# Kernel optimization log

Measured on AMD Instinct MI355X. Metric: run time of the kernel, lower is better.

The kernel has to match this reference:

```python
import jax, jax.numpy as jnp
import numpy as np

N, L, H, V = 64, 512, 1024, 32000


def setup_inputs() -> dict:
    key = jax.random.key(0)
    k1, k2, k3, k4, k5, k6 = jax.random.split(key, 6)
    s = 1.0 / np.sqrt(H)
    return {
        "x": jax.random.randint(k1, (N, L), 0, V, dtype=jnp.int32),
        "emb": jax.random.normal(k2, (V, H), dtype=jnp.float32) * 0.02,
        "W_hh_w": jax.random.normal(k3, (H, H), dtype=jnp.float32) * s,
        "W_hh_b": jax.random.normal(k4, (H,), dtype=jnp.float32) * s,
        "W_xh_w": jax.random.normal(k5, (H, H), dtype=jnp.float32) * s,
        "W_xh_b": jax.random.normal(k6, (H,), dtype=jnp.float32) * s,
    }


def reference(x, emb, W_hh_w, W_hh_b, W_xh_w, W_xh_b):
    # h_t = tanh(W_hh h_{t-1} + b_hh + W_xh e_t + b_xh); returns (N, L, H)
    now = emb[x]                                    # (N, L, H) embedding lookup
    # W_xh part has no recurrence: precompute for all steps at once.
    xh = jnp.einsum("nlh,oh->nlo", now, W_xh_w) + W_xh_b + W_hh_b  # (N, L, H)

    def step(h, xh_t):
        h = jnp.tanh(h @ W_hh_w.T + xh_t)           # (N, H)
        return h, h

    h0 = jnp.zeros((x.shape[0], W_hh_w.shape[0]), dtype=emb.dtype)
    _, memories = jax.lax.scan(step, h0, jnp.swapaxes(xh, 0, 1))  # (L, N, H)
    return jnp.swapaxes(memories, 0, 1)             # (N, L, H)
```

## Files before the change

kernel.cpp:

```cpp
#include <hip/hip_runtime.h>
#include <math.h>

typedef _Float16 half8 __attribute__((ext_vector_type(8)));
typedef _Float16 half4 __attribute__((ext_vector_type(4)));
typedef float floatx4 __attribute__((ext_vector_type(4)));
typedef unsigned long long u64;

#define NB 64
#define LQ 512
#define HD 1024

__device__ inline half8 cvt2(const float4 a, const float4 b) {
  half8 h;
  h[0]=(_Float16)a.x; h[1]=(_Float16)a.y; h[2]=(_Float16)a.z; h[3]=(_Float16)a.w;
  h[4]=(_Float16)b.x; h[5]=(_Float16)b.y; h[6]=(_Float16)b.z; h[7]=(_Float16)b.w;
  return h;
}

__device__ inline floatx4 ld_sc16(const void* p) {
  floatx4 r;
  asm volatile("global_load_dwordx4 %0, %1, off sc0 sc1"
               : "=v"(r) : "v"(p) : "memory");
  return r;
}
__device__ inline void st_sc16(void* p, floatx4 v) {
  asm volatile("global_store_dwordx4 %0, %1, off sc0 sc1"
               :: "v"(p), "v"(v) : "memory");
}
__device__ inline void st_flag(int* p, int v) {
  __hip_atomic_store(p, v, __ATOMIC_RELAXED, __HIP_MEMORY_SCOPE_SYSTEM);
}
__device__ inline void vmcnt0() { asm volatile("s_waitcnt vmcnt(0)" ::: "memory"); }

__device__ inline float ftanh(float x) {
  float e = __expf(2.0f * x);
  return 1.0f - 2.0f / (e + 1.0f);
}

__global__ __launch_bounds__(256) void gemm1_kernel(
    const int* __restrict__ x, const float* __restrict__ emb,
    const float* __restrict__ Wxh, const float* __restrict__ bxh,
    const float* __restrict__ bhh, float* __restrict__ out)
{
  __shared__ alignas(16) _Float16 As[128][72];
  __shared__ alignas(16) _Float16 Bs[128][72];
  const int tid  = threadIdx.x;
  const int lane = tid & 63, wv = tid >> 6;
  const int wm = wv & 1, wn = wv >> 1;
  const int Mbase = blockIdx.x * 128;
  const int Nbase = blockIdx.y * 128;

  const int srow  = tid >> 1;
  const int shalf = tid & 1;
  const size_t erow = (size_t)x[Mbase + srow] * HD;
  const size_t brow = (size_t)(Nbase + srow) * HD;

  floatx4 acc[4][4];
#pragma unroll
  for (int i = 0; i < 4; i++)
#pragma unroll
    for (int j = 0; j < 4; j++) acc[i][j] = (floatx4)0.f;

  for (int c = 0; c < 16; ++c) {
    const int k0 = c * 64 + shalf * 32;
    const float4* ap = (const float4*)(emb + erow + k0);
    const float4* bp = (const float4*)(Wxh + brow + k0);
    float4 av[8], bv[8];
#pragma unroll
    for (int i = 0; i < 8; i++) { av[i] = ap[i]; bv[i] = bp[i]; }
    __syncthreads();
#pragma unroll
    for (int i = 0; i < 4; i++) {
      *(half8*)&As[srow][shalf*32 + i*8] = cvt2(av[2*i], av[2*i+1]);
      *(half8*)&Bs[srow][shalf*32 + i*8] = cvt2(bv[2*i], bv[2*i+1]);
    }
    __syncthreads();
#pragma unroll
    for (int s = 0; s < 2; ++s) {
      const int koff = s*32 + (lane >> 4) * 8;
      half8 af[4], bf[4];
#pragma unroll
      for (int i = 0; i < 4; i++) {
        af[i] = *(const half8*)&As[wm*64 + i*16 + (lane & 15)][koff];
        bf[i] = *(const half8*)&Bs[wn*64 + i*16 + (lane & 15)][koff];
      }
#pragma unroll
      for (int i = 0; i < 4; i++)
#pragma unroll
        for (int j = 0; j < 4; j++)
          acc[i][j] = __builtin_amdgcn_mfma_f32_16x16x32_f16(af[i], bf[j], acc[i][j], 0, 0, 0);
    }
  }
#pragma unroll
  for (int j = 0; j < 4; j++) {
    const int o = Nbase + wn*64 + j*16 + (lane & 15);
    const float bias = bxh[o] + bhh[o];
#pragma unroll
    for (int i = 0; i < 4; i++) {
      const int mb = Mbase + wm*64 + i*16 + ((lane >> 4) * 4);
#pragma unroll
      for (int r = 0; r < 4; r++)
        out[(size_t)(mb + r) * HD + o] = acc[i][j][r] + bias;
    }
  }
}

__global__ __launch_bounds__(256, 1) void rnn_kernel(
    const float* __restrict__ Whh, float* __restrict__ out,
    char* __restrict__ hb, int* __restrict__ flags)
{
  __shared__ alignas(16) _Float16 Ws[32 * 1024];
  __shared__ alignas(16) _Float16 Tls[4 * 16 * 40];
  const int tid = threadIdx.x, lane = tid & 63, w = tid >> 6;
  const int j = blockIdx.x, obase = j * 32;
  const int col = lane & 15, quad = lane >> 4;
  const int wid = j * 4 + w;

  {
    const int o = tid >> 3, t8 = tid & 7;
    const float* src = Whh + (size_t)(obase + o) * HD;
#pragma unroll
    for (int i = 0; i < 16; ++i) {
      const int c16 = t8 * 16 + i;
      float4 v0 = *(const float4*)(src + c16 * 8);
      float4 v1 = *(const float4*)(src + c16 * 8 + 4);
      *(half8*)&Ws[o * 1024 + ((c16 ^ (o & 7)) * 8)] = cvt2(v0, v1);
    }
  }
  __syncthreads();

  const int n = 16 * w + col;
  _Float16* Tw = &Tls[w * 640];
  float* outp = out + (size_t)n * LQ * HD + obase + quad * 4;
  u64* fl64 = (u64*)flags;
  char* hbw = hb + (size_t)w * 32768 + (size_t)lane * 16;

  for (int t = 0; t < LQ; ++t) {
    const float* xp = outp + (size_t)t * HD;
    floatx4 xv0 = *(const floatx4*)xp;
    floatx4 xv1 = *(const floatx4*)(xp + 16);
    floatx4 acc0 = (floatx4)0.f, acc1 = (floatx4)0.f;

    if (t > 0) {
      int spins = 0;
      for (;;) {
        u64 v = __hip_atomic_load(&fl64[lane], __ATOMIC_RELAXED, __HIP_MEMORY_SCOPE_SYSTEM);
        int lo = (int)(unsigned)v, hi = (int)(v >> 32);
        if (__all(lo >= t && hi >= t)) break;
        if (++spins > (1 << 20)) break;
      }

      const char* blk = hbw + (size_t)((t - 1) & 1) * 131072;
      floatx4 hv[32];
#pragma unroll
      for (int c = 0; c < 32; ++c) hv[c] = ld_sc16(blk + c * 1024);

      floatx4 a0a = (floatx4)0.f, a1a = (floatx4)0.f;
      floatx4 a0b = (floatx4)0.f, a1b = (floatx4)0.f;
      asm volatile("s_waitcnt vmcnt(16)" ::: "memory");
      __builtin_amdgcn_sched_barrier(0);
#pragma unroll
      for (int c = 0; c < 16; ++c) {
        const int sw = ((4 * c + quad) ^ (col & 7)) * 8;
        half8 b0 = *(const half8*)&Ws[col * 1024 + sw];
        half8 b1 = *(const half8*)&Ws[(16 + col) * 1024 + sw];
        half8 hf = __builtin_bit_cast(half8, hv[c]);
        a0a = __builtin_amdgcn_mfma_f32_16x16x32_f16(b0, hf, a0a, 0, 0, 0);
        a1a = __builtin_amdgcn_mfma_f32_16x16x32_f16(b1, hf, a1a, 0, 0, 0);
      }
      vmcnt0();
      __builtin_amdgcn_sched_barrier(0);
#pragma unroll
      for (int c = 16; c < 32; ++c) {
        const int sw = ((4 * c + quad) ^ (col & 7)) * 8;
        half8 b0 = *(const half8*)&Ws[col * 1024 + sw];
        half8 b1 = *(const half8*)&Ws[(16 + col) * 1024 + sw];
        half8 hf = __builtin_bit_cast(half8, hv[c]);
        a0b = __builtin_amdgcn_mfma_f32_16x16x32_f16(b0, hf, a0b, 0, 0, 0);
        a1b = __builtin_amdgcn_mfma_f32_16x16x32_f16(b1, hf, a1b, 0, 0, 0);
      }
      acc0 = a0a + a0b;
      acc1 = a1a + a1b;
    }

    floatx4 h0, h1;
    half4 p0, p1;
#pragma unroll
    for (int r = 0; r < 4; ++r) {
      h0[r] = ftanh(acc0[r] + xv0[r]);
      h1[r] = ftanh(acc1[r] + xv1[r]);
      p0[r] = (_Float16)h0[r];
      p1[r] = (_Float16)h1[r];
    }

    *(half4*)&Tw[col * 40 + quad * 4] = p0;
    *(half4*)&Tw[col * 40 + 16 + quad * 4] = p1;
    __builtin_amdgcn_wave_barrier();
    asm volatile("s_waitcnt lgkmcnt(0)" ::: "memory");
    floatx4 myc = *(const floatx4*)&Tw[col * 40 + quad * 8];

    st_sc16(hb + (size_t)(t & 1) * 131072 + (size_t)w * 32768 +
            (size_t)j * 1024 + (size_t)lane * 16, myc);
    vmcnt0();
    if (lane == 0) st_flag(&flags[wid], t + 1);

    float* op = outp + (size_t)t * HD;
    *(floatx4*)op = h0;
    *(floatx4*)(op + 16) = h1;
  }
}

extern "C" void kernel_launch(void* const* d_in, const int* in_sizes, int n_in,
                              void* d_out, int out_size, void* d_ws, size_t ws_size,
                              hipStream_t stream) {
  const int*   x   = (const int*)d_in[0];
  const float* emb = (const float*)d_in[1];
  const float* Whh = (const float*)d_in[2];
  const float* bhh = (const float*)d_in[3];
  const float* Wxh = (const float*)d_in[4];
  const float* bxh = (const float*)d_in[5];
  float* out = (float*)d_out;

  char* hbuf = (char*)d_ws;
  int*  fl   = (int*)((char*)d_ws + 262144);

  gemm1_kernel<<<dim3(256, 8), 256, 0, stream>>>(x, emb, Wxh, bxh, bhh, out);
  rnn_kernel<<<dim3(32), 256, 0, stream>>>(Whh, out, hbuf, fl);
}
```

Measured before the change: 3.526 ms.

## Replace flag-based step sync with sentinel-tagged hidden-state buffers

Drops the per-wave flag publish and spin loop. Consumers instead poll the hidden-state data itself, which is quad-buffered and pre-filled with a sentinel value (initialised in the GEMM kernel and re-armed two steps ahead). Producers write fp16 results straight from registers with two 8-byte system-scope stores, skipping the LDS transpose and the vmcnt wait before the flag store. This removes one round trip (data store, wait, flag store, flag poll) per timestep. The cost is re-polling loads for chunks that are not ready yet, and correctness relies on a real fp16 data pattern never equalling the sentinel and on store ordering within each 4-byte word.

```diff
diff --git a/kernel.cpp b/kernel.cpp
--- a/kernel.cpp
+++ b/kernel.cpp
@@ -4,11 +4,13 @@
 typedef _Float16 half8 __attribute__((ext_vector_type(8)));
 typedef _Float16 half4 __attribute__((ext_vector_type(4)));
 typedef float floatx4 __attribute__((ext_vector_type(4)));
-typedef unsigned long long u64;
+typedef float floatx2 __attribute__((ext_vector_type(2)));
+typedef unsigned int uintx4 __attribute__((ext_vector_type(4)));
 
 #define NB 64
 #define LQ 512
 #define HD 1024
+#define SENT 0x7E7E7E7Eu
 
 __device__ inline half8 cvt2(const float4 a, const float4 b) {
   half8 h;
@@ -17,18 +19,20 @@
   return h;
 }
 
-__device__ inline floatx4 ld_sc16(const void* p) {
+__device__ inline floatx4 ld_sys16(const void* p) {
   floatx4 r;
   asm volatile("global_load_dwordx4 %0, %1, off sc0 sc1"
                : "=v"(r) : "v"(p) : "memory");
   return r;
 }
-__device__ inline void st_sc16(void* p, floatx4 v) {
-  asm volatile("global_store_dwordx4 %0, %1, off sc0 sc1"
+__device__ inline void st_sys8x2(void* p, floatx2 a, floatx2 b) {
+  asm volatile("global_store_dwordx2 %0, %1, off sc0 sc1\n\t"
+               "global_store_dwordx2 %0, %2, off offset:512 sc0 sc1"
+               :: "v"(p), "v"(a), "v"(b) : "memory");
+}
+__device__ inline void st_sys4(void* p, unsigned v) {
+  asm volatile("global_store_dword %0, %1, off sc0 sc1"
                :: "v"(p), "v"(v) : "memory");
-}
-__device__ inline void st_flag(int* p, int v) {
-  __hip_atomic_store(p, v, __ATOMIC_RELAXED, __HIP_MEMORY_SCOPE_SYSTEM);
 }
 __device__ inline void vmcnt0() { asm volatile("s_waitcnt vmcnt(0)" ::: "memory"); }
 
@@ -40,8 +44,15 @@
 __global__ __launch_bounds__(256) void gemm1_kernel(
     const int* __restrict__ x, const float* __restrict__ emb,
     const float* __restrict__ Wxh, const float* __restrict__ bxh,
-    const float* __restrict__ bhh, float* __restrict__ out)
+    const float* __restrict__ bhh, float* __restrict__ out,
+    char* __restrict__ hb)
 {
+  {
+    const int bid = blockIdx.y * gridDim.x + blockIdx.x;
+    if (threadIdx.x < 64)
+      st_sys4((unsigned*)hb + (size_t)bid * 64 + threadIdx.x, SENT);
+  }
+
   __shared__ alignas(16) _Float16 As[128][72];
   __shared__ alignas(16) _Float16 Bs[128][72];
   const int tid  = threadIdx.x;
@@ -107,14 +118,12 @@
 
 __global__ __launch_bounds__(256, 1) void rnn_kernel(
     const float* __restrict__ Whh, float* __restrict__ out,
-    char* __restrict__ hb, int* __restrict__ flags)
+    char* __restrict__ hb)
 {
   __shared__ alignas(16) _Float16 Ws[32 * 1024];
-  __shared__ alignas(16) _Float16 Tls[4 * 16 * 40];
   const int tid = threadIdx.x, lane = tid & 63, w = tid >> 6;
   const int j = blockIdx.x, obase = j * 32;
   const int col = lane & 15, quad = lane >> 4;
-  const int wid = j * 4 + w;
 
   {
     const int o = tid >> 3, t8 = tid & 7;
@@ -130,10 +139,11 @@
   __syncthreads();
 
   const int n = 16 * w + col;
-  _Float16* Tw = &Tls[w * 640];
   float* outp = out + (size_t)n * LQ * HD + obase + quad * 4;
-  u64* fl64 = (u64*)flags;
   char* hbw = hb + (size_t)w * 32768 + (size_t)lane * 16;
+  char* pubb = hb + (size_t)w * 32768 + (size_t)j * 1024 +
+               (size_t)((quad >> 1) * 256 + col * 16 + (quad & 1) * 8);
+  const floatx2 sent2 = __builtin_bit_cast(floatx2, (unsigned long long)SENT << 32 | SENT);
 
   for (int t = 0; t < LQ; ++t) {
     const float* xp = outp + (size_t)t * HD;
@@ -142,42 +152,40 @@
     floatx4 acc0 = (floatx4)0.f, acc1 = (floatx4)0.f;
 
     if (t > 0) {
-      int spins = 0;
-      for (;;) {
-        u64 v = __hip_atomic_load(&fl64[lane], __ATOMIC_RELAXED, __HIP_MEMORY_SCOPE_SYSTEM);
-        int lo = (int)(unsigned)v, hi = (int)(v >> 32);
-        if (__all(lo >= t && hi >= t)) break;
-        if (++spins > (1 << 20)) break;
-      }
-
-      const char* blk = hbw + (size_t)((t - 1) & 1) * 131072;
+      const char* blk = hbw + (size_t)((t - 1) & 3) * 131072;
       floatx4 hv[32];
-#pragma unroll
-      for (int c = 0; c < 32; ++c) hv[c] = ld_sc16(blk + c * 1024);
+      unsigned need = 0xFFFFFFFFu;
+      int sweeps = 0;
+      do {
+#pragma unroll
+        for (int c = 0; c < 32; ++c)
+          if (need & (1u << c)) hv[c] = ld_sys16(blk + c * 1024);
+        vmcnt0();
+        __builtin_amdgcn_sched_barrier(0);
+#pragma unroll
+        for (int c = 0; c < 32; ++c)
+          if (need & (1u << c)) {
+            uintx4 u = __builtin_bit_cast(uintx4, hv[c]);
+            if ((u[0] != SENT) & (u[1] != SENT) & (u[2] != SENT) & (u[3] != SENT))
+              need &= ~(1u << c);
+          }
+      } while (need != 0 && ++sweeps < 4096);
 
       floatx4 a0a = (floatx4)0.f, a1a = (floatx4)0.f;
       floatx4 a0b = (floatx4)0.f, a1b = (floatx4)0.f;
-      asm volatile("s_waitcnt vmcnt(16)" ::: "memory");
-      __builtin_amdgcn_sched_barrier(0);
-#pragma unroll
-      for (int c = 0; c < 16; ++c) {
+#pragma unroll
+      for (int c = 0; c < 32; ++c) {
         const int sw = ((4 * c + quad) ^ (col & 7)) * 8;
         half8 b0 = *(const half8*)&Ws[col * 1024 + sw];
         half8 b1 = *(const half8*)&Ws[(16 + col) * 1024 + sw];
         half8 hf = __builtin_bit_cast(half8, hv[c]);
-        a0a = __builtin_amdgcn_mfma_f32_16x16x32_f16(b0, hf, a0a, 0, 0, 0);
-        a1a = __builtin_amdgcn_mfma_f32_16x16x32_f16(b1, hf, a1a, 0, 0, 0);
-      }
-      vmcnt0();
-      __builtin_amdgcn_sched_barrier(0);
-#pragma unroll
-      for (int c = 16; c < 32; ++c) {
-        const int sw = ((4 * c + quad) ^ (col & 7)) * 8;
-        half8 b0 = *(const half8*)&Ws[col * 1024 + sw];
-        half8 b1 = *(const half8*)&Ws[(16 + col) * 1024 + sw];
-        half8 hf = __builtin_bit_cast(half8, hv[c]);
-        a0b = __builtin_amdgcn_mfma_f32_16x16x32_f16(b0, hf, a0b, 0, 0, 0);
-        a1b = __builtin_amdgcn_mfma_f32_16x16x32_f16(b1, hf, a1b, 0, 0, 0);
+        if (c & 1) {
+          a0b = __builtin_amdgcn_mfma_f32_16x16x32_f16(b0, hf, a0b, 0, 0, 0);
+          a1b = __builtin_amdgcn_mfma_f32_16x16x32_f16(b1, hf, a1b, 0, 0, 0);
+        } else {
+          a0a = __builtin_amdgcn_mfma_f32_16x16x32_f16(b0, hf, a0a, 0, 0, 0);
+          a1a = __builtin_amdgcn_mfma_f32_16x16x32_f16(b1, hf, a1a, 0, 0, 0);
+        }
       }
       acc0 = a0a + a0b;
       acc1 = a1a + a1b;
@@ -193,16 +201,10 @@
       p1[r] = (_Float16)h1[r];
     }
 
-    *(half4*)&Tw[col * 40 + quad * 4] = p0;
-    *(half4*)&Tw[col * 40 + 16 + quad * 4] = p1;
-    __builtin_amdgcn_wave_barrier();
-    asm volatile("s_waitcnt lgkmcnt(0)" ::: "memory");
-    floatx4 myc = *(const floatx4*)&Tw[col * 40 + quad * 8];
-
-    st_sc16(hb + (size_t)(t & 1) * 131072 + (size_t)w * 32768 +
-            (size_t)j * 1024 + (size_t)lane * 16, myc);
-    vmcnt0();
-    if (lane == 0) st_flag(&flags[wid], t + 1);
+    st_sys8x2(pubb + (size_t)(t & 3) * 131072,
+              __builtin_bit_cast(floatx2, p0), __builtin_bit_cast(floatx2, p1));
+
+    st_sys8x2(pubb + (size_t)((t + 2) & 3) * 131072, sent2, sent2);
 
     float* op = outp + (size_t)t * HD;
     *(floatx4*)op = h0;
@@ -222,8 +224,7 @@
   float* out = (float*)d_out;
 
   char* hbuf = (char*)d_ws;
-  int*  fl   = (int*)((char*)d_ws + 262144);
-
-  gemm1_kernel<<<dim3(256, 8), 256, 0, stream>>>(x, emb, Wxh, bxh, bhh, out);
-  rnn_kernel<<<dim3(32), 256, 0, stream>>>(Whh, out, hbuf, fl);
-}
+
+  gemm1_kernel<<<dim3(256, 8), 256, 0, stream>>>(x, emb, Wxh, bxh, bhh, out, hbuf);
+  rnn_kernel<<<dim3(32), 256, 0, stream>>>(Whh, out, hbuf);
+}
```

Measured after the change: 3.725 ms. 5.6% more time.
